# Kernel tuning notes

Hardware: AMD Instinct MI355X
Metric: run time of the kernel (lower is better)

Reference implementation:

```python
import math
import jax, jax.numpy as jnp
import numpy as np

HEADS = 8
D_MODEL = 256


def positional_encoding_2d(c, h, w):
    # faithful port of wzlxjtu/PositionalEncoding2D
    d = c // 2
    div_term = jnp.exp(jnp.arange(0.0, d, 2, dtype=jnp.float32) * (-(math.log(10000.0) / d)))  # [d//2? no: d/2 entries -> d//2]
    pos_w = jnp.arange(0.0, w, dtype=jnp.float32)[:, None] * div_term  # [w, d//2]
    pos_h = jnp.arange(0.0, h, dtype=jnp.float32)[:, None] * div_term  # [h, d//2]
    pe = jnp.zeros((c, h, w), dtype=jnp.float32)
    sw = jnp.broadcast_to(jnp.sin(pos_w).T[:, None, :], (div_term.shape[0], h, w))
    cw = jnp.broadcast_to(jnp.cos(pos_w).T[:, None, :], (div_term.shape[0], h, w))
    sh = jnp.broadcast_to(jnp.sin(pos_h).T[:, :, None], (div_term.shape[0], h, w))
    ch = jnp.broadcast_to(jnp.cos(pos_h).T[:, :, None], (div_term.shape[0], h, w))
    pe = pe.at[0:d:2].set(sw)
    pe = pe.at[1:d:2].set(cw)
    pe = pe.at[d::2].set(sh)
    pe = pe.at[d + 1::2].set(ch)
    return pe


def setup_inputs() -> dict:
    key = jax.random.key(0)
    ks = jax.random.split(key, 9)
    b, c, h, w = 2, D_MODEL, 64, 64
    x = jax.random.normal(ks[0], (b, c, h, w), dtype=jnp.float32)
    s = 0.02
    Wq = jax.random.normal(ks[1], (c, c), dtype=jnp.float32) * s
    Wk = jax.random.normal(ks[2], (c, c), dtype=jnp.float32) * s
    Wv = jax.random.normal(ks[3], (c, c), dtype=jnp.float32) * s
    Wo = jax.random.normal(ks[4], (c, c), dtype=jnp.float32) * s
    bq = jax.random.normal(ks[5], (c,), dtype=jnp.float32) * s
    bk = jax.random.normal(ks[6], (c,), dtype=jnp.float32) * s
    bv = jax.random.normal(ks[7], (c,), dtype=jnp.float32) * s
    bo = jax.random.normal(ks[8], (c,), dtype=jnp.float32) * s
    return {"x": x, "Wq": Wq, "bq": bq, "Wk": Wk, "bk": bk,
            "Wv": Wv, "bv": bv, "Wo": Wo, "bo": bo}


def reference(x, Wq, bq, Wk, bk, Wv, bv, Wo, bo):
    b, c, h, w = x.shape
    dk = c // HEADS
    pe = positional_encoding_2d(c, h, w)
    x2 = x + pe[None]                                   # [b,c,h,w]
    tok = x2.reshape(b, c, h * w).transpose(0, 2, 1)    # [b,N,c]
    q = (tok @ Wq.T + bq).reshape(b, -1, HEADS, dk).transpose(0, 2, 1, 3)  # [b,H,N,dk]
    k = (tok @ Wk.T + bk).reshape(b, -1, HEADS, dk).transpose(0, 2, 1, 3)
    v = (tok @ Wv.T + bv).reshape(b, -1, HEADS, dk).transpose(0, 2, 1, 3)
    scores = jnp.einsum('bhnd,bhmd->bhnm', q, k) / math.sqrt(dk)  # [b,H,N,N]
    attn = jax.nn.softmax(scores, axis=-1)
    out = jnp.einsum('bhnm,bhmd->bhnd', attn, v)        # [b,H,N,dk]
    concat = out.transpose(0, 2, 1, 3).reshape(b, -1, c)  # [b,N,c]
    proj = concat @ Wo.T + bo                           # [b,N,c]
    return proj.transpose(0, 2, 1).reshape(b, c, h, w)
```

## Files before the change

### kernel.cpp

```cpp
#include <hip/hip_runtime.h>
#include <hip/hip_bf16.h>
#include <cstdint>

typedef float f32x4 __attribute__((ext_vector_type(4)));
typedef __bf16 bf16x8 __attribute__((ext_vector_type(8)));
typedef __bf16 bf16x4 __attribute__((ext_vector_type(4)));
typedef __bf16 bf16x2 __attribute__((ext_vector_type(2)));
typedef short short4v __attribute__((ext_vector_type(4)));
typedef uint32_t uint2v __attribute__((ext_vector_type(2)));

#define MFMA_K32(A, B, C) __builtin_amdgcn_mfma_f32_16x16x32_bf16((A), (B), (C), 0, 0, 0)

#if __has_builtin(__builtin_amdgcn_mfma_f32_16x16x16bf16_1k)
#define MFMA_K16(A, B, C) __builtin_amdgcn_mfma_f32_16x16x16bf16_1k((A), (B), (C), 0, 0, 0)
#elif __has_builtin(__builtin_amdgcn_mfma_f32_16x16x16_bf16)
static __device__ __forceinline__ f32x4 mfma_k16_alt(short4v a, short4v b, f32x4 c) {
    return __builtin_amdgcn_mfma_f32_16x16x16_bf16(*(bf16x4*)&a, *(bf16x4*)&b, c, 0, 0, 0);
}
#define MFMA_K16(A, B, C) mfma_k16_alt((A), (B), (C))
#else
#define MFMA_K16(A, B, C) (C)
#endif

#if __has_builtin(__builtin_amdgcn_exp2f)
#define EXP2(x) __builtin_amdgcn_exp2f(x)
#else
#define EXP2(x) exp2f(x)
#endif

static __device__ __forceinline__ uint16_t f2b(float f) {
    uint32_t u = __float_as_uint(f);
    uint32_t r = (u + 0x7fffu + ((u >> 16) & 1u)) >> 16;
    return (uint16_t)r;
}

static __device__ __forceinline__ uint32_t packbf(float a, float b) {
#if __has_builtin(__builtin_amdgcn_cvt_pk_bf16_f32)
    bf16x2 v = __builtin_amdgcn_cvt_pk_bf16_f32(a, b);
    return *(uint32_t*)&v;
#else
    uint32_t ua = __float_as_uint(a);
    ua += 0x7fffu + ((ua >> 16) & 1u);
    uint32_t ub = __float_as_uint(b);
    ub += 0x7fffu + ((ub >> 16) & 1u);
    return __builtin_amdgcn_perm(ub, ua, 0x07060302);
#endif
}

__global__ __launch_bounds__(256) void wconv_pe(const float* __restrict__ wq,
                                                const float* __restrict__ wk,
                                                const float* __restrict__ wv,
                                                const float* __restrict__ wo,
                                                uint16_t* __restrict__ dst,
                                                float* __restrict__ pet) {
    int bid = blockIdx.x, t = threadIdx.x;
    if (bid < 1024) {
        int idx = bid * 256 + t;
        int which = idx >> 16, off = idx & 65535;
        const float* s = (which == 0) ? wq : (which == 1) ? wk : (which == 2) ? wv : wo;
        dst[idx] = f2b(s[off]);
    } else {
        int idx = (bid - 1024) * 256 + t;
        int cc = idx >> 6, p = idx & 63;
        int i = (cc & 127) >> 1;
        float dt = __expf((float)(2 * i) * -0.07195578415606394f);
        float sv, cv;
        __sincosf((float)p * dt, &sv, &cv);
        pet[idx] = (cc & 1) ? cv : sv;
    }
}

__global__ __launch_bounds__(256) void peadd(const float* __restrict__ x,
                                             const float* __restrict__ pet,
                                             uint16_t* __restrict__ tok) {
    __shared__ uint16_t T[64][65];
    int t = threadIdx.x, bid = blockIdx.x;
    int nt = bid & 63, ct = (bid >> 6) & 3, bb = bid >> 8;
    int n0 = nt << 6, c0 = ct << 6;
    int nl = t & 63, cq = t >> 6;
    int n = n0 + nl;
    int posh = n0 >> 6;
#pragma unroll
    for (int p = 0; p < 16; ++p) {
        int cl = cq * 16 + p;
        int cc = c0 + cl;
        float pe = pet[cc * 64 + ((cc & 128) ? posh : nl)];
        T[cl][nl] = f2b(x[((size_t)(bb * 256 + cc) << 12) + n] + pe);
    }
    __syncthreads();
#pragma unroll
    for (int p = 0; p < 16; ++p) {
        int tl = cq * 16 + p;
        tok[(((size_t)(bb << 12) | (n0 + tl)) << 8) + c0 + nl] = T[nl][tl];
    }
}

__global__ __launch_bounds__(256) void qkv_gemm(const uint16_t* __restrict__ tok,
                                                const uint16_t* __restrict__ Wall,
                                                const float* __restrict__ bq,
                                                const float* __restrict__ bk,
                                                const float* __restrict__ bv,
                                                uint16_t* __restrict__ qo,
                                                uint16_t* __restrict__ ko,
                                                uint16_t* __restrict__ vo) {
    __shared__ __align__(16) uint16_t WS[64][264];
    int tid = threadIdx.x, wv = tid >> 6, lane = tid & 63;
    int c16 = lane & 15, quad = lane >> 4;
    int M0 = blockIdx.x * 64 + wv * 16;
    int O0 = blockIdx.y * 64;
    const uint16_t* arow = tok + (size_t)(M0 + c16) * 256;
    bf16x8 af[8];
#pragma unroll
    for (int kk = 0; kk < 8; ++kk) af[kk] = *(const bf16x8*)(arow + kk * 32 + quad * 8);
    f32x4 zero = {0.f, 0.f, 0.f, 0.f};
    int bb = M0 >> 12, n = (M0 + c16) & 4095;
    int srow = tid >> 5, sch = (tid & 31) << 3;
    for (int mat = 0; mat < 3; ++mat) {
        const uint16_t* Wg = Wall + (size_t)mat * 65536 + (size_t)O0 * 256;
        __syncthreads();
#pragma unroll
        for (int p = 0; p < 8; ++p)
            *(bf16x8*)(&WS[p * 8 + srow][sch]) = *(const bf16x8*)(Wg + (p * 8 + srow) * 256 + sch);
        __syncthreads();
        f32x4 acc[4] = {zero, zero, zero, zero};
#pragma unroll
        for (int kk = 0; kk < 8; ++kk) {
            int k0 = kk * 32 + quad * 8;
#pragma unroll
            for (int nb = 0; nb < 4; ++nb)
                acc[nb] = MFMA_K32(*(const bf16x8*)(&WS[nb * 16 + c16][k0]),
                                   af[kk], acc[nb]);
        }
        const float* bias = (mat == 0) ? bq : (mat == 1) ? bk : bv;
        if (mat < 2) {
            float scale = (mat == 0) ? 0.25505654134660127f : 1.0f;
            uint16_t* dst = (mat == 0) ? qo : ko;
#pragma unroll
            for (int nb = 0; nb < 4; ++nb) {
                int o = O0 + nb * 16 + quad * 4;
                f32x4 bi = *(const f32x4*)(bias + o);
                int h = o >> 5, dd = o & 31;
                uint2v pk;
                pk[0] = packbf((acc[nb][0] + bi[0]) * scale, (acc[nb][1] + bi[1]) * scale);
                pk[1] = packbf((acc[nb][2] + bi[2]) * scale, (acc[nb][3] + bi[3]) * scale);
                *(uint2v*)(dst + ((size_t)(bb * 8 + h) * 4096 + n) * 32 + dd) = pk;
            }
        } else {
#pragma unroll
            for (int nb = 0; nb < 4; ++nb)
#pragma unroll
                for (int r = 0; r < 4; ++r) {
                    int o = O0 + nb * 16 + quad * 4 + r;
                    vo[((size_t)(bb * 8 + (o >> 5)) * 32 + (o & 31)) * 4096 + n] =
                        f2b(acc[nb][r] + bias[o]);
                }
        }
    }
}

static __device__ __forceinline__ void attn_qblock(const bf16x8 (&kf)[4],
                                                   const short4v (&vf)[2][4],
                                                   bf16x8 qf, f32x4& oA, f32x4& oB,
                                                   f32x4& oS) {
    f32x4 zero = {0.f, 0.f, 0.f, 0.f};
    const short4v ones = {0x3F80, 0x3F80, 0x3F80, 0x3F80};
    f32x4 s[4];
#pragma unroll
    for (int kc = 0; kc < 4; ++kc) s[kc] = MFMA_K32(kf[kc], qf, zero);
#pragma unroll
    for (int kc = 0; kc < 4; ++kc) {
#pragma unroll
        for (int r = 0; r < 4; ++r) s[kc][r] = EXP2(s[kc][r]);
        union { short4v s4; uint32_t u[2]; } pa;
        pa.u[0] = packbf(s[kc][0], s[kc][1]);
        pa.u[1] = packbf(s[kc][2], s[kc][3]);
        oA = MFMA_K16(pa.s4, vf[0][kc], oA);
        oB = MFMA_K16(pa.s4, vf[1][kc], oB);
        oS = MFMA_K16(pa.s4, ones, oS);
    }
}

__global__ __launch_bounds__(512, 4) void flash(const uint16_t* __restrict__ qb,
                                                const uint16_t* __restrict__ kb,
                                                const uint16_t* __restrict__ vtb,
                                                uint16_t* __restrict__ concat) {
    __shared__ __align__(16) char smem[38912];
    int tid = threadIdx.x, wv = tid >> 6, lane = tid & 63;
    int c16 = lane & 15, quad = lane >> 4;
    int half = tid >> 8, t2 = tid & 255;
    int bh = blockIdx.y;
    int q0 = (blockIdx.x << 7) + (wv & 3) * 32;
    size_t base = (size_t)bh << 12;

    uint16_t* KT = (uint16_t*)(smem + half * 19456);
    uint16_t* VT = (uint16_t*)(smem + half * 19456 + 10240);

    const uint16_t* kgp = kb + (base + (size_t)half * 2048 + (t2 >> 2)) * 32 + (t2 & 3) * 8;
    const uint16_t* vgp = vtb + ((size_t)bh * 32 + (t2 >> 3)) * 4096 + half * 2048 + (t2 & 7) * 8;
    uint16_t* kls = KT + (t2 >> 2) * 40 + (t2 & 3) * 8;
    uint16_t* vls = VT + (t2 >> 3) * 72 + (t2 & 7) * 8;

    bf16x8 qf0 = *(const bf16x8*)(qb + (base + q0 + c16) * 32 + quad * 8);
    bf16x8 qf1 = *(const bf16x8*)(qb + (base + q0 + 16 + c16) * 32 + quad * 8);

    f32x4 zero = {0.f, 0.f, 0.f, 0.f};
    f32x4 o00 = zero, o01 = zero, o10 = zero, o11 = zero;
    f32x4 oS0 = zero, oS1 = zero;

    {
        bf16x8 kr = *(const bf16x8*)kgp;
        bf16x8 vr = *(const bf16x8*)vgp;
        *(bf16x8*)kls = kr;
        *(bf16x8*)vls = vr;
    }
    __syncthreads();

    for (int kt = 0; kt < 32; ++kt) {
        int cur = kt & 1;
        int kn = (kt + 1) & 31;
        bf16x8 kr = *(const bf16x8*)(kgp + (size_t)kn * 2048);
        bf16x8 vr = *(const bf16x8*)(vgp + kn * 64);
        const uint16_t* kfp = KT + cur * 2560 + c16 * 40 + quad * 8;
        const uint16_t* vfp = VT + cur * 2304 + c16 * 72 + quad * 4;
        bf16x8 kf[4];
        short4v vf[2][4];
#pragma unroll
        for (int kc = 0; kc < 4; ++kc) kf[kc] = *(const bf16x8*)(kfp + kc * 640);
#pragma unroll
        for (int kc = 0; kc < 4; ++kc) {
            vf[0][kc] = *(const short4v*)(vfp + kc * 16);
            vf[1][kc] = *(const short4v*)(vfp + 1152 + kc * 16);
        }
        attn_qblock(kf, vf, qf0, o00, o01, oS0);
        attn_qblock(kf, vf, qf1, o10, o11, oS1);
        *(bf16x8*)(kls + (cur ^ 1) * 2560) = kr;
        *(bf16x8*)(vls + (cur ^ 1) * 2304) = vr;
        __syncthreads();
    }

    float* ov = (float*)smem;
    if (wv >= 4) {
        float* d = ov + ((wv - 4) * 64 + lane) * 25;
#pragma unroll
        for (int r = 0; r < 4; ++r) {
            d[r] = o00[r]; d[4 + r] = o01[r]; d[8 + r] = o10[r]; d[12 + r] = o11[r];
            d[16 + r] = oS0[r]; d[20 + r] = oS1[r];
        }
    }
    __syncthreads();
    if (wv < 4) {
        const float* s = ov + (wv * 64 + lane) * 25;
#pragma unroll
        for (int r = 0; r < 4; ++r) {
            o00[r] += s[r]; o01[r] += s[4 + r]; o10[r] += s[8 + r]; o11[r] += s[12 + r];
            oS0[r] += s[16 + r]; oS1[r] += s[20 + r];
        }
        int h = bh & 7, bb = bh >> 3;
#pragma unroll
        for (int r = 0; r < 4; ++r) {
            float i0 = 1.f / oS0[r];
            float i1 = 1.f / oS1[r];
            int n = q0 + quad * 4 + r;
            size_t row0 = ((size_t)bb * 4096 + n) * 256 + h * 32;
            size_t row1 = ((size_t)bb * 4096 + n + 16) * 256 + h * 32;
            concat[row0 + c16]      = f2b(o00[r] * i0);
            concat[row0 + 16 + c16] = f2b(o01[r] * i0);
            concat[row1 + c16]      = f2b(o10[r] * i1);
            concat[row1 + 16 + c16] = f2b(o11[r] * i1);
        }
    }
}

__global__ __launch_bounds__(256) void proj_gemm(const uint16_t* __restrict__ concat,
                                                 const uint16_t* __restrict__ Wo,
                                                 const float* __restrict__ bo,
                                                 float* __restrict__ out) {
    __shared__ __align__(16) uint16_t WS[64][264];
    int tid = threadIdx.x, wv = tid >> 6, lane = tid & 63;
    int c16 = lane & 15, quad = lane >> 4;
    int M0 = blockIdx.x * 64 + wv * 16;
    int O0 = blockIdx.y * 64;
    int srow = tid >> 5, sch = (tid & 31) << 3;
    const uint16_t* Wg = Wo + (size_t)O0 * 256;
#pragma unroll
    for (int p = 0; p < 8; ++p)
        *(bf16x8*)(&WS[p * 8 + srow][sch]) = *(const bf16x8*)(Wg + (p * 8 + srow) * 256 + sch);
    const uint16_t* crow = concat + (size_t)(M0 + c16) * 256;
    bf16x8 af[8];
#pragma unroll
    for (int kk = 0; kk < 8; ++kk) af[kk] = *(const bf16x8*)(crow + kk * 32 + quad * 8);
    __syncthreads();
    f32x4 zero = {0.f, 0.f, 0.f, 0.f};
    f32x4 acc[4] = {zero, zero, zero, zero};
#pragma unroll
    for (int kk = 0; kk < 8; ++kk) {
        int k0 = kk * 32 + quad * 8;
#pragma unroll
        for (int nb = 0; nb < 4; ++nb)
            acc[nb] = MFMA_K32(*(const bf16x8*)(&WS[nb * 16 + c16][k0]),
                               af[kk], acc[nb]);
    }
    int bb = M0 >> 12, n = (M0 + c16) & 4095;
#pragma unroll
    for (int nb = 0; nb < 4; ++nb)
#pragma unroll
        for (int r = 0; r < 4; ++r) {
            int o = O0 + nb * 16 + quad * 4 + r;
            out[((size_t)(bb * 256 + o) << 12) + n] = acc[nb][r] + bo[o];
        }
}

extern "C" void kernel_launch(void* const* d_in, const int* in_sizes, int n_in,
                              void* d_out, int out_size, void* d_ws, size_t ws_size,
                              hipStream_t stream) {
    const float* x  = (const float*)d_in[0];
    const float* Wq = (const float*)d_in[1];
    const float* bq = (const float*)d_in[2];
    const float* Wk = (const float*)d_in[3];
    const float* bk = (const float*)d_in[4];
    const float* Wv = (const float*)d_in[5];
    const float* bv = (const float*)d_in[6];
    const float* Wo = (const float*)d_in[7];
    const float* bo = (const float*)d_in[8];
    float* out = (float*)d_out;

    uint16_t* ws   = (uint16_t*)d_ws;
    uint16_t* Wb   = ws;
    uint16_t* tok  = Wb + 4 * 65536;
    uint16_t* q    = tok + 2097152;
    uint16_t* k    = q + 2097152;
    uint16_t* vt   = k + 2097152;
    uint16_t* cc   = vt + 2097152;
    float*    pet  = (float*)(cc + 2097152);

    wconv_pe<<<1088, 256, 0, stream>>>(Wq, Wk, Wv, Wo, Wb, pet);
    peadd<<<512, 256, 0, stream>>>(x, pet, tok);
    qkv_gemm<<<dim3(128, 4), 256, 0, stream>>>(tok, Wb, bq, bk, bv, q, k, vt);
    flash<<<dim3(32, 16), 512, 0, stream>>>(q, k, vt, cc);
    proj_gemm<<<dim3(128, 4), 256, 0, stream>>>(cc, Wb + 3 * 65536, bo, out);
}
```

Measured before the change: 150.3 us.

## Use K=32 bf16 MFMA for PV product with permuted key rows

```diff
diff --git a/kernel.cpp b/kernel.cpp
--- a/kernel.cpp
+++ b/kernel.cpp
@@ -4,23 +4,10 @@
 
 typedef float f32x4 __attribute__((ext_vector_type(4)));
 typedef __bf16 bf16x8 __attribute__((ext_vector_type(8)));
-typedef __bf16 bf16x4 __attribute__((ext_vector_type(4)));
 typedef __bf16 bf16x2 __attribute__((ext_vector_type(2)));
-typedef short short4v __attribute__((ext_vector_type(4)));
 typedef uint32_t uint2v __attribute__((ext_vector_type(2)));
 
 #define MFMA_K32(A, B, C) __builtin_amdgcn_mfma_f32_16x16x32_bf16((A), (B), (C), 0, 0, 0)
-
-#if __has_builtin(__builtin_amdgcn_mfma_f32_16x16x16bf16_1k)
-#define MFMA_K16(A, B, C) __builtin_amdgcn_mfma_f32_16x16x16bf16_1k((A), (B), (C), 0, 0, 0)
-#elif __has_builtin(__builtin_amdgcn_mfma_f32_16x16x16_bf16)
-static __device__ __forceinline__ f32x4 mfma_k16_alt(short4v a, short4v b, f32x4 c) {
-    return __builtin_amdgcn_mfma_f32_16x16x16_bf16(*(bf16x4*)&a, *(bf16x4*)&b, c, 0, 0, 0);
-}
-#define MFMA_K16(A, B, C) mfma_k16_alt((A), (B), (C))
-#else
-#define MFMA_K16(A, B, C) (C)
-#endif
 
 #if __has_builtin(__builtin_amdgcn_exp2f)
 #define EXP2(x) __builtin_amdgcn_exp2f(x)
@@ -159,24 +146,29 @@
 }
 
 static __device__ __forceinline__ void attn_qblock(const bf16x8 (&kf)[4],
-                                                   const short4v (&vf)[2][4],
-                                                   bf16x8 qf, f32x4& oA, f32x4& oB,
-                                                   f32x4& oS) {
+                                                   const bf16x8 (&vA)[2],
+                                                   const bf16x8 (&vB)[2],
+                                                   bf16x8 ones, bf16x8 qf,
+                                                   f32x4& oA, f32x4& oB, f32x4& oS) {
     f32x4 zero = {0.f, 0.f, 0.f, 0.f};
-    const short4v ones = {0x3F80, 0x3F80, 0x3F80, 0x3F80};
     f32x4 s[4];
 #pragma unroll
-    for (int kc = 0; kc < 4; ++kc) s[kc] = MFMA_K32(kf[kc], qf, zero);
-#pragma unroll
-    for (int kc = 0; kc < 4; ++kc) {
-#pragma unroll
-        for (int r = 0; r < 4; ++r) s[kc][r] = EXP2(s[kc][r]);
-        union { short4v s4; uint32_t u[2]; } pa;
-        pa.u[0] = packbf(s[kc][0], s[kc][1]);
-        pa.u[1] = packbf(s[kc][2], s[kc][3]);
-        oA = MFMA_K16(pa.s4, vf[0][kc], oA);
-        oB = MFMA_K16(pa.s4, vf[1][kc], oB);
-        oS = MFMA_K16(pa.s4, ones, oS);
+    for (int c = 0; c < 4; ++c) s[c] = MFMA_K32(kf[c], qf, zero);
+#pragma unroll
+    for (int p = 0; p < 2; ++p) {
+#pragma unroll
+        for (int r = 0; r < 4; ++r) {
+            s[2 * p][r] = EXP2(s[2 * p][r]);
+            s[2 * p + 1][r] = EXP2(s[2 * p + 1][r]);
+        }
+        union { bf16x8 v; uint32_t u[4]; } pa;
+        pa.u[0] = packbf(s[2 * p][0], s[2 * p][1]);
+        pa.u[1] = packbf(s[2 * p][2], s[2 * p][3]);
+        pa.u[2] = packbf(s[2 * p + 1][0], s[2 * p + 1][1]);
+        pa.u[3] = packbf(s[2 * p + 1][2], s[2 * p + 1][3]);
+        oA = MFMA_K32(pa.v, vA[p], oA);
+        oB = MFMA_K32(pa.v, vB[p], oB);
+        oS = MFMA_K32(pa.v, ones, oS);
     }
 }
 
@@ -184,7 +176,7 @@
                                                 const uint16_t* __restrict__ kb,
                                                 const uint16_t* __restrict__ vtb,
                                                 uint16_t* __restrict__ concat) {
-    __shared__ __align__(16) char smem[38912];
+    __shared__ __align__(16) char smem[43008];
     int tid = threadIdx.x, wv = tid >> 6, lane = tid & 63;
     int c16 = lane & 15, quad = lane >> 4;
     int half = tid >> 8, t2 = tid & 255;
@@ -192,16 +184,23 @@
     int q0 = (blockIdx.x << 7) + (wv & 3) * 32;
     size_t base = (size_t)bh << 12;
 
-    uint16_t* KT = (uint16_t*)(smem + half * 19456);
-    uint16_t* VT = (uint16_t*)(smem + half * 19456 + 10240);
+    uint16_t* KT = (uint16_t*)(smem + half * 21504);
+    uint16_t* VT = (uint16_t*)(smem + half * 21504 + 12288);
 
     const uint16_t* kgp = kb + (base + (size_t)half * 2048 + (t2 >> 2)) * 32 + (t2 & 3) * 8;
     const uint16_t* vgp = vtb + ((size_t)bh * 32 + (t2 >> 3)) * 4096 + half * 2048 + (t2 & 7) * 8;
-    uint16_t* kls = KT + (t2 >> 2) * 40 + (t2 & 3) * 8;
+    uint16_t* kls = KT + (t2 >> 2) * 48 + (t2 & 3) * 8;
     uint16_t* vls = VT + (t2 >> 3) * 72 + (t2 & 7) * 8;
 
     bf16x8 qf0 = *(const bf16x8*)(qb + (base + q0 + c16) * 32 + quad * 8);
     bf16x8 qf1 = *(const bf16x8*)(qb + (base + q0 + 16 + c16) * 32 + quad * 8);
+
+    int rbase = ((c16 >> 2) << 3) + (c16 & 3);
+
+    union { uint32_t u[4]; bf16x8 v; } onesu;
+    onesu.u[0] = 0x3F803F80u; onesu.u[1] = 0x3F803F80u;
+    onesu.u[2] = 0x3F803F80u; onesu.u[3] = 0x3F803F80u;
+    bf16x8 ones = onesu.v;
 
     f32x4 zero = {0.f, 0.f, 0.f, 0.f};
     f32x4 o00 = zero, o01 = zero, o10 = zero, o11 = zero;
@@ -220,20 +219,20 @@
         int kn = (kt + 1) & 31;
         bf16x8 kr = *(const bf16x8*)(kgp + (size_t)kn * 2048);
         bf16x8 vr = *(const bf16x8*)(vgp + kn * 64);
-        const uint16_t* kfp = KT + cur * 2560 + c16 * 40 + quad * 8;
-        const uint16_t* vfp = VT + cur * 2304 + c16 * 72 + quad * 4;
-        bf16x8 kf[4];
-        short4v vf[2][4];
-#pragma unroll
-        for (int kc = 0; kc < 4; ++kc) kf[kc] = *(const bf16x8*)(kfp + kc * 640);
-#pragma unroll
-        for (int kc = 0; kc < 4; ++kc) {
-            vf[0][kc] = *(const short4v*)(vfp + kc * 16);
-            vf[1][kc] = *(const short4v*)(vfp + 1152 + kc * 16);
-        }
-        attn_qblock(kf, vf, qf0, o00, o01, oS0);
-        attn_qblock(kf, vf, qf1, o10, o11, oS1);
-        *(bf16x8*)(kls + (cur ^ 1) * 2560) = kr;
+        const uint16_t* kfp = KT + cur * 3072 + rbase * 48 + quad * 8;
+        const uint16_t* vfp = VT + cur * 2304 + c16 * 72 + quad * 8;
+        bf16x8 kf[4], vA[2], vB[2];
+        kf[0] = *(const bf16x8*)(kfp);
+        kf[1] = *(const bf16x8*)(kfp + 192);
+        kf[2] = *(const bf16x8*)(kfp + 1536);
+        kf[3] = *(const bf16x8*)(kfp + 1536 + 192);
+        vA[0] = *(const bf16x8*)(vfp);
+        vA[1] = *(const bf16x8*)(vfp + 32);
+        vB[0] = *(const bf16x8*)(vfp + 1152);
+        vB[1] = *(const bf16x8*)(vfp + 1152 + 32);
+        attn_qblock(kf, vA, vB, ones, qf0, o00, o01, oS0);
+        attn_qblock(kf, vA, vB, ones, qf1, o10, o11, oS1);
+        *(bf16x8*)(kls + (cur ^ 1) * 3072) = kr;
         *(bf16x8*)(vls + (cur ^ 1) * 2304) = vr;
         __syncthreads();
     }
```

Result: no change. 150.3 us (+0.0%).
